# Kernel optimization log

Measured on AMD Instinct MI355X. Metric: run time of the kernel, lower is better.

The kernel has to match this reference:

```python
import jax, jax.numpy as jnp
import numpy as np

DN = ('NCHW', 'OIHW', 'NCHW')


def conv(x, w, s, p):
    return jax.lax.conv_general_dilated(x, w, (s, s), [(p, p), (p, p)], dimension_numbers=DN)


def batchnorm(x, g, b, eps=1e-5):
    # torch BatchNorm2d in training mode: biased batch stats over (N,H,W)
    mu = jnp.mean(x, (0, 2, 3), keepdims=True)
    var = jnp.var(x, (0, 2, 3), keepdims=True)
    return (x - mu) * jax.lax.rsqrt(var + eps) * g.reshape(1, -1, 1, 1) + b.reshape(1, -1, 1, 1)


def pconv(x, mask, W, b, s, p, gb, act):
    # PartialConvLayer.forward
    k = W.shape[-1]
    y = conv(x * mask, W, s, p)
    mc = conv(mask, jnp.ones((1, 1, k, k), x.dtype), s, p)  # all-ones mask conv (frozen)
    zero = mc == 0
    msum = jnp.where(zero, 1.0, mc)
    if b is not None:
        bias = b.reshape(1, -1, 1, 1)
        y = (y - bias) / msum + bias
    else:
        y = y / msum
    y = jnp.where(zero, 0.0, y)
    new_mask = jnp.where(zero, 0.0, 1.0).astype(x.dtype)
    if gb is not None:
        y = batchnorm(y, gb[0], gb[1])
    if act == 'relu':
        y = jax.nn.relu(y)
    elif act == 'leaky':
        y = jnp.where(y >= 0, y, 0.2 * y)
    return y, new_mask


def nlm(mask, feat, h2):
    # Vectorized batch_NLM: Nadaraya-Watson estimator between miss and bkg pixels.
    # Equivalent to the original triple loop: for each miss pixel i,
    #   out[i] = sum_j exp(-||x_i-x_j||^2/h^2) x_j / sum_j exp(-...)   over bkg j.
    # Subtracting the per-row min distance before exp is mathematically identical
    # (the factor cancels in the ratio) and numerically stable.
    bs, C, H, W = feat.shape
    N = H * W
    x = feat.transpose(0, 2, 3, 1).reshape(bs, N, C)
    bkg = mask.reshape(bs, N) > 0.5
    sq = jnp.sum(x * x, -1)  # [bs,N]
    D = jnp.maximum(sq[:, :, None] + sq[:, None, :] - 2.0 * jnp.einsum('bic,bjc->bij', x, x), 0.0)
    Dm = jnp.where(bkg[:, None, :], D, jnp.inf)
    dmin = jnp.min(Dm, -1, keepdims=True)
    w = jnp.where(bkg[:, None, :], jnp.exp(-(D - dmin) / h2), 0.0)
    avg = jnp.einsum('bij,bjc->bic', w, x) / jnp.sum(w, -1, keepdims=True)
    out = jnp.where(bkg[:, :, None], x, avg)  # only miss pixels are replaced
    return out.reshape(bs, H, W, C).transpose(0, 3, 1, 2)


def up2(x):
    return jnp.repeat(jnp.repeat(x, 2, axis=2), 2, axis=3)


def forward(input_x, mask, enc1_W, enc2_W, enc3_W, enc4_W, dec4_W, dec3_W, dec2_W, dec1_W, dec1_b,
            enc2_g, enc2_b, enc3_g, enc3_b, enc4_g, enc4_b,
            dec4_g, dec4_b, dec3_g, dec3_b, dec2_g, dec2_b):
    H_GAUSS2 = 25.0  # h_gaussian = 5
    h0, m0 = input_x, mask
    h1, m1 = pconv(h0, m0, enc1_W, None, 2, 3, None, 'relu')                 # down-7, bn=False
    h2, m2 = pconv(h1, m1, enc2_W, None, 2, 2, (enc2_g, enc2_b), 'relu')     # down-5
    # NLM feature swapping at layer 2 (torch code detaches -> stop_gradient)
    h2 = jax.lax.stop_gradient(nlm(m2, h2, H_GAUSS2))
    buffer_swapped = h2
    h3, m3 = pconv(h2, m2, enc3_W, None, 2, 1, (enc3_g, enc3_b), 'relu')     # down-3
    h4, m4 = pconv(h3, m3, enc4_W, None, 2, 1, (enc4_g, enc4_b), 'relu')     # down-3

    out, omask = h4, m4
    out, omask = up2(out), up2(omask)
    out, omask = pconv(jnp.concatenate([out, h3], 1), omask, dec4_W, None, 1, 1, (dec4_g, dec4_b), 'leaky')
    out, omask = up2(out), up2(omask)
    out, omask = pconv(jnp.concatenate([out, buffer_swapped], 1), omask, dec3_W, None, 1, 1, (dec3_g, dec3_b), 'leaky')
    out, omask = up2(out), up2(omask)
    out, omask = pconv(jnp.concatenate([out, h1], 1), omask, dec2_W, None, 1, 1, (dec2_g, dec2_b), 'leaky')
    out, omask = up2(out), up2(omask)
    out, omask = pconv(jnp.concatenate([out, h0], 1), omask, dec1_W, dec1_b, 1, 1, None, 'none')  # bn=False, bias, no act
    return out


def setup_inputs() -> dict:
    key = jax.random.key(0)
    ks = jax.random.split(key, 12)

    def kaiming(k, shape):
        fan_in = shape[1] * shape[2] * shape[3]
        return jax.random.normal(k, shape, jnp.float32) * np.float32(np.sqrt(2.0 / fan_in))

    bs = 8
    input_x = jax.random.normal(ks[0], (bs, 128, 144, 144), jnp.float32)
    # mask: 1 = background (valid), 0 = missing. Hole large enough to survive two downsamples.
    mask = jnp.ones((bs, 1, 144, 144), jnp.float32).at[:, :, 40:96, 40:96].set(0.0)

    inp = {
        'input_x': input_x,
        'mask': mask,
        'enc1_W': kaiming(ks[1], (256, 128, 7, 7)),
        'enc2_W': kaiming(ks[2], (512, 256, 5, 5)),
        'enc3_W': kaiming(ks[3], (512, 512, 3, 3)),
        'enc4_W': kaiming(ks[4], (512, 512, 3, 3)),
        'dec4_W': kaiming(ks[5], (512, 1024, 3, 3)),
        'dec3_W': kaiming(ks[6], (512, 1024, 3, 3)),
        'dec2_W': kaiming(ks[7], (256, 768, 3, 3)),
        'dec1_W': kaiming(ks[8], (128, 384, 3, 3)),
        'dec1_b': jnp.zeros((128,), jnp.float32),
    }
    for name, c in [('enc2', 512), ('enc3', 512), ('enc4', 512), ('dec4', 512), ('dec3', 512), ('dec2', 256)]:
        inp[name + '_g'] = jnp.ones((c,), jnp.float32)
        inp[name + '_b'] = jnp.zeros((c,), jnp.float32)
    return inp


def reference(input_x, mask, enc1_W, enc2_W, enc3_W, enc4_W, dec4_W, dec3_W, dec2_W, dec1_W, dec1_b,
              enc2_g, enc2_b, enc3_g, enc3_b, enc4_g, enc4_b,
              dec4_g, dec4_b, dec3_g, dec3_b, dec2_g, dec2_b):
    return forward(input_x, mask, enc1_W, enc2_W, enc3_W, enc4_W, dec4_W, dec3_W, dec2_W, dec1_W, dec1_b,
                   enc2_g, enc2_b, enc3_g, enc3_b, enc4_g, enc4_b,
                   dec4_g, dec4_b, dec3_g, dec3_b, dec2_g, dec2_b)
```

## Files before the change

### kernel.cpp

```cpp
#include <hip/hip_runtime.h>
#include <math.h>

#define ACT_NONE 0
#define ACT_RELU 1
#define ACT_LEAKY 2

#define EPI_F32 0
#define EPI_PAIR_RELU 1
#define EPI_F32_BIAS 2

typedef __attribute__((ext_vector_type(8))) short short8;
typedef __attribute__((ext_vector_type(8))) __bf16 bf16x8;
typedef __attribute__((ext_vector_type(4))) float f32x4;
typedef __attribute__((ext_vector_type(4))) unsigned uint4v;

__device__ __forceinline__ float actf(float y, int act) {
    if (act == ACT_RELU)  return y > 0.f ? y : 0.f;
    if (act == ACT_LEAKY) return y >= 0.f ? y : 0.2f * y;
    return y;
}

__device__ __forceinline__ unsigned f2bf_rne(float f) {
    unsigned u = __float_as_uint(f);
    return (u + 0x7FFFu + ((u >> 16) & 1u)) >> 16;
}
__device__ __forceinline__ float bf2f(unsigned h) { return __uint_as_float(h << 16); }
__device__ __forceinline__ unsigned splitpack(float f) {
    unsigned hi = f2bf_rne(f);
    float r = f - bf2f(hi);
    unsigned lo = f2bf_rne(r);
    return (hi & 0xFFFFu) | (lo << 16);
}

__device__ __forceinline__ f32x4 mfma16(short8 a, short8 b, f32x4 c) {
    return __builtin_amdgcn_mfma_f32_16x16x32_bf16(
        __builtin_bit_cast(bf16x8, a), __builtin_bit_cast(bf16x8, b), c, 0, 0, 0);
}

template<int K, int S, bool MHALF>
__global__ void maskconv_kernel(const float* __restrict__ M, int HM, int WM,
                                float* __restrict__ mc, float* __restrict__ nm,
                                int N, int Hin, int Win, int Hout, int Wout) {
    constexpr int P = (K - 1) / 2;
    int idx = blockIdx.x * blockDim.x + threadIdx.x;
    int total = N * Hout * Wout;
    if (idx >= total) return;
    int wo = idx % Wout;
    int t  = idx / Wout;
    int ho = t % Hout;
    int n  = t / Hout;
    float s = 0.f;
    for (int kh = 0; kh < K; ++kh) {
        int ih = ho * S - P + kh;
        if ((unsigned)ih >= (unsigned)Hin) continue;
        const float* mrow = M + ((size_t)n * HM + (MHALF ? (ih >> 1) : ih)) * WM;
        for (int kw = 0; kw < K; ++kw) {
            int iw = wo * S - P + kw;
            if ((unsigned)iw < (unsigned)Win)
                s += mrow[MHALF ? (iw >> 1) : iw];
        }
    }
    mc[idx] = s;
    nm[idx] = (s == 0.f) ? 0.f : 1.f;
}

__global__ void wtransform(const float* __restrict__ W, short* __restrict__ Whi,
                           short* __restrict__ Wlo, int Cout, int Cin, int Ksz,
                           size_t total) {
    size_t idx = (size_t)blockIdx.x * blockDim.x + threadIdx.x;
    if (idx >= total) return;
    int j = (int)(idx & 7);
    int lane = (int)((idx >> 3) & 63);
    size_t r = idx >> 9;
    int COB = Cout >> 4, KB = Cin >> 5;
    int cob = (int)(r % COB); r /= COB;
    int kb = (int)(r % KB);
    int tap = (int)(r / KB);
    int co = cob * 16 + (lane & 15);
    int ci = kb * 32 + (lane >> 4) * 8 + j;
    float f = W[((size_t)co * Cin + ci) * Ksz + tap];
    unsigned hi = f2bf_rne(f);
    float rr = f - bf2f(hi);
    unsigned lo = f2bf_rne(rr);
    Whi[idx] = (short)hi;
    Wlo[idx] = (short)lo;
}

template<int K, int S, int TH, int TW, int NFW, bool AF32, int EPI>
__global__ __launch_bounds__(512) void conv_enc(
    const void* __restrict__ Asrc, int Cin, int Hin, int Win,
    const float* __restrict__ M,
    const short* __restrict__ Whi, const short* __restrict__ Wlo,
    const float* __restrict__ mc, const float* __restrict__ bias,
    void* __restrict__ outp,
    int Hout, int Wout, int Cout, int TX)
{
    static_assert(S == 2, "parity layout assumes stride 2");
    constexpr int P = (K - 1) / 2;
    constexpr int HH  = (TH - 1) * S + K;
    constexpr int HWC = (TW - 1) * S + K;
    constexpr int PXC = HH * HWC;
    constexpr int PW  = (HWC + 1) / 2;
    constexpr int PXC2 = HH * PW * 2;
    __shared__ __align__(16) unsigned BH[4 * PXC2 * 4];
    __shared__ __align__(16) unsigned BL[4 * PXC2 * 4];

    const int t    = threadIdx.x;
    const int lane = t & 63;
    const int wv   = t >> 6;
    const int wm   = wv >> 1;
    const int wn   = wv & 1;
    const int img  = blockIdx.z;
    const int coB  = blockIdx.y * 256;
    const int tile = blockIdx.x;
    const int ty   = tile / TX, tx = tile - ty * TX;
    const int oy0  = ty * TH, ox0 = tx * TW;
    const int KB   = Cin >> 5;
    const int COB  = Cout >> 4;
    const size_t HW = (size_t)Hin * Win;
    const int g  = lane >> 4;
    const int pl = lane & 15;

    f32x4 acc[4][NFW] = {};

#pragma unroll 1
    for (int kb = 0; kb < KB; ++kb) {
        for (int q = t; q < PXC; q += 512) {
            const int r = q / HWC, c = q - r * HWC;
            const int qq = r * PW + (c >> 1) + (c & 1) * (HH * PW);
            const int iy = oy0 * S - P + r;
            const int ix = ox0 * S - P + c;
            bool sel = (unsigned)iy < (unsigned)Hin && (unsigned)ix < (unsigned)Win;
            size_t base = 0;
            if (sel) {
                sel = M[(size_t)img * HW + (size_t)iy * Win + ix] != 0.f;
                base = (size_t)img * Cin * HW + (size_t)iy * Win + ix;
            }
#pragma unroll
            for (int gg = 0; gg < 4; ++gg) {
                const int c0 = kb * 32 + gg * 8;
                unsigned v[8];
#pragma unroll
                for (int j = 0; j < 8; ++j) v[j] = 0u;
                if (sel) {
                    if (AF32) {
                        const float* s = (const float*)Asrc + base + (size_t)c0 * HW;
#pragma unroll
                        for (int j = 0; j < 8; ++j) v[j] = splitpack(s[(size_t)j * HW]);
                    } else {
                        const unsigned* s = (const unsigned*)Asrc + base + (size_t)c0 * HW;
#pragma unroll
                        for (int j = 0; j < 8; ++j) v[j] = s[(size_t)j * HW];
                    }
                }
                uint4v hd, ld;
#pragma unroll
                for (int j = 0; j < 4; ++j) {
                    hd[j] = (v[2 * j] & 0xFFFFu) | (v[2 * j + 1] << 16);
                    ld[j] = (v[2 * j] >> 16) | (v[2 * j + 1] & 0xFFFF0000u);
                }
                *(uint4v*)&BH[(gg * PXC2 + qq) * 4] = hd;
                *(uint4v*)&BL[(gg * PXC2 + qq) * 4] = ld;
            }
        }
        __syncthreads();

#pragma unroll 1
        for (int kh = 0; kh < K; ++kh)
#pragma unroll 1
        for (int kw = 0; kw < K; ++kw) {
            const int tap = kh * K + kw;
            const size_t wb = (((size_t)tap * KB + kb) * COB + (coB >> 4) + wm * 4) * 512
                            + (size_t)lane * 8;
            short8 ah[4], al[4];
#pragma unroll
            for (int fm = 0; fm < 4; ++fm) {
                ah[fm] = *(const short8*)(Whi + wb + (size_t)fm * 512);
                al[fm] = *(const short8*)(Wlo + wb + (size_t)fm * 512);
            }
#pragma unroll
            for (int fn = 0; fn < NFW; ++fn) {
                const int pxf = (wn * NFW + fn) * 16 + pl;
                const int oy = pxf / TW, ox = pxf - oy * TW;
                const int qq = (oy * S + kh) * PW + ox + (kw >> 1) + (kw & 1) * (HH * PW);
                short8 bh = *(const short8*)&BH[(g * PXC2 + qq) * 4];
                short8 bl = *(const short8*)&BL[(g * PXC2 + qq) * 4];
#pragma unroll
                for (int fm = 0; fm < 4; ++fm) {
                    acc[fm][fn] = mfma16(ah[fm], bh, acc[fm][fn]);
                    acc[fm][fn] = mfma16(al[fm], bh, acc[fm][fn]);
                    acc[fm][fn] = mfma16(ah[fm], bl, acc[fm][fn]);
                }
            }
        }
        __syncthreads();
    }

    const int Npix = Hout * Wout;
    const float* mcb = mc + (size_t)img * Npix;
#pragma unroll
    for (int fm = 0; fm < 4; ++fm)
#pragma unroll
    for (int fn = 0; fn < NFW; ++fn) {
        const int co = coB + (wm * 4 + fm) * 16 + (lane >> 4) * 4;
        const int pxf = (wn * NFW + fn) * 16 + (lane & 15);
        const int oy = pxf / TW, ox = pxf - oy * TW;
        const int gy = oy0 + oy, gx = ox0 + ox;
        if (gy >= Hout || gx >= Wout) continue;
        const float m = mcb[(size_t)gy * Wout + gx];
        f32x4 a = acc[fm][fn];
#pragma unroll
        for (int r = 0; r < 4; ++r) {
            float y = a[r];
            if (EPI == EPI_F32_BIAS) {
                const float bv = bias[co + r];
                y = (m == 0.f) ? 0.f : (y - bv) / m + bv;
            } else {
                y = (m == 0.f) ? 0.f : y / m;
            }
            const size_t oidx = ((size_t)img * Cout + co + r) * Npix + (size_t)gy * Wout + gx;
            if (EPI == EPI_PAIR_RELU) {
                y = y > 0.f ? y : 0.f;
                ((unsigned*)outp)[oidx] = splitpack(y);
            } else {
                ((float*)outp)[oidx] = y;
            }
        }
    }
}

template<int TH, int TW, int NFW, bool BF32, int EPI>
__global__ __launch_bounds__(512) void conv3x3(
    const void* __restrict__ Asrc, int CA, int HA, int WA,
    const void* __restrict__ Bsrc, int CB,
    const float* __restrict__ M,
    const short* __restrict__ Whi, const short* __restrict__ Wlo,
    const float* __restrict__ mc, const float* __restrict__ bias,
    void* __restrict__ outp,
    int Hout, int Wout, int Cout, int TX)
{
    constexpr int HALO_H = TH + 2, HALO_W = TW + 2, HALO = HALO_H * HALO_W;
    constexpr int NPIX = TH * TW;
    static_assert(NPIX == 64 * NFW, "tile must be 64*NFW pixels");
    __shared__ __align__(16) unsigned BH[4 * HALO * 4];
    __shared__ __align__(16) unsigned BL[4 * HALO * 4];

    const int t    = threadIdx.x;
    const int lane = t & 63;
    const int wv   = t >> 6;
    const int wm   = wv & 1;
    const int wn   = wv >> 1;
    const int img  = blockIdx.z;
    const int coB  = blockIdx.y * 128;
    const int tile = blockIdx.x;
    const int ty   = tile / TX;
    const int tx   = tile - ty * TX;
    const int oy0  = ty * TH, ox0 = tx * TW;
    const int Cin  = CA + CB;
    const int KB   = Cin >> 5;
    const int COB  = Cout >> 4;
    const int WM   = Wout >> 1;
    const size_t HWA = (size_t)HA * WA;
    const size_t HWB = (size_t)Hout * Wout;

    const int sg = t >> 7;
    const int st = t & 127;
    const int g  = lane >> 4;
    const int pl = lane & 15;

    f32x4 acc[4][NFW] = {};
    const size_t wstride = (size_t)KB * COB * 512;

#pragma unroll 1
    for (int kb = 0; kb < KB; ++kb) {
        for (int q = st; q < HALO; q += 128) {
            const int hy = q / HALO_W, hx = q - hy * HALO_W;
            const int iy = oy0 - 1 + hy, ix = ox0 - 1 + hx;
            bool sel = false;
            size_t abase = 0, bbase = 0;
            if ((unsigned)iy < (unsigned)Hout && (unsigned)ix < (unsigned)Wout) {
                sel = M[((size_t)img * (Hout >> 1) + (iy >> 1)) * WM + (ix >> 1)] != 0.f;
                if (sel) {
                    abase = (size_t)img * CA * HWA + (size_t)(iy >> 1) * WA + (ix >> 1);
                    bbase = (size_t)img * CB * HWB + (size_t)iy * Wout + ix;
                }
            }
            const int c = kb * 32 + sg * 8;
            unsigned v[8];
#pragma unroll
            for (int j = 0; j < 8; ++j) v[j] = 0u;
            if (sel) {
                if (c < CA) {
                    const unsigned* s = (const unsigned*)Asrc + abase + (size_t)c * HWA;
#pragma unroll
                    for (int j = 0; j < 8; ++j) v[j] = s[(size_t)j * HWA];
                } else {
                    if (BF32) {
                        const float* s = (const float*)Bsrc + bbase + (size_t)(c - CA) * HWB;
#pragma unroll
                        for (int j = 0; j < 8; ++j) v[j] = splitpack(s[(size_t)j * HWB]);
                    } else {
                        const unsigned* s = (const unsigned*)Bsrc + bbase + (size_t)(c - CA) * HWB;
#pragma unroll
                        for (int j = 0; j < 8; ++j) v[j] = s[(size_t)j * HWB];
                    }
                }
            }
            uint4v hd, ld;
#pragma unroll
            for (int j = 0; j < 4; ++j) {
                hd[j] = (v[2 * j] & 0xFFFFu) | (v[2 * j + 1] << 16);
                ld[j] = (v[2 * j] >> 16) | (v[2 * j + 1] & 0xFFFF0000u);
            }
            *(uint4v*)&BH[(sg * HALO + q) * 4] = hd;
            *(uint4v*)&BL[(sg * HALO + q) * 4] = ld;
        }
        __syncthreads();

        size_t wb = ((size_t)kb * COB + (coB >> 4) + wm * 4) * 512 + (size_t)lane * 8;
#pragma unroll 1
        for (int tap = 0; tap < 9; ++tap) {
            const int dh = tap / 3, dw = tap - dh * 3;
            short8 ah[4], al[4];
#pragma unroll
            for (int fm = 0; fm < 4; ++fm) {
                ah[fm] = *(const short8*)(Whi + wb + (size_t)fm * 512);
                al[fm] = *(const short8*)(Wlo + wb + (size_t)fm * 512);
            }
#pragma unroll
            for (int fn = 0; fn < NFW; ++fn) {
                const int pxf = (wn * NFW + fn) * 16 + pl;
                const int oy = pxf / TW, ox = pxf - oy * TW;
                const int hpx = (oy + dh) * HALO_W + (ox + dw);
                short8 bh = *(const short8*)&BH[(g * HALO + hpx) * 4];
                short8 bl = *(const short8*)&BL[(g * HALO + hpx) * 4];
#pragma unroll
                for (int fm = 0; fm < 4; ++fm) {
                    acc[fm][fn] = mfma16(ah[fm], bh, acc[fm][fn]);
                    acc[fm][fn] = mfma16(al[fm], bh, acc[fm][fn]);
                    acc[fm][fn] = mfma16(ah[fm], bl, acc[fm][fn]);
                }
            }
            wb += wstride;
        }
        __syncthreads();
    }

    const float* mcb = mc + (size_t)img * HWB;
#pragma unroll
    for (int fm = 0; fm < 4; ++fm)
#pragma unroll
    for (int fn = 0; fn < NFW; ++fn) {
        const int co = coB + (wm * 4 + fm) * 16 + (lane >> 4) * 4;
        const int pxf = (wn * NFW + fn) * 16 + (lane & 15);
        const int oy = pxf / TW, ox = pxf - oy * TW;
        const int gy = oy0 + oy, gx = ox0 + ox;
        if (gy >= Hout || gx >= Wout) continue;
        const float m = mcb[(size_t)gy * Wout + gx];
        f32x4 a = acc[fm][fn];
#pragma unroll
        for (int r = 0; r < 4; ++r) {
            float y = a[r];
            if (EPI == EPI_F32_BIAS) {
                const float bv = bias[co + r];
                y = (m == 0.f) ? 0.f : (y - bv) / m + bv;
            } else {
                y = (m == 0.f) ? 0.f : y / m;
            }
            ((float*)outp)[((size_t)img * Cout + co + r) * HWB + (size_t)gy * Wout + gx] = y;
        }
    }
}

__global__ __launch_bounds__(256) void bn_stats_kernel(const float* __restrict__ y,
                                                       int N, int C, int HW,
                                                       float* __restrict__ mean,
                                                       float* __restrict__ istd) {
    const int c = blockIdx.x;
    double s = 0.0, s2 = 0.0;
    const int tot = N * HW;
    for (int i = threadIdx.x; i < tot; i += blockDim.x) {
        int n = i / HW, hw = i - n * HW;
        float v = y[((size_t)n * C + c) * HW + hw];
        s += v;
        s2 += (double)v * v;
    }
    __shared__ double sh[256], sh2[256];
    sh[threadIdx.x] = s; sh2[threadIdx.x] = s2;
    __syncthreads();
    for (int o = 128; o > 0; o >>= 1) {
        if (threadIdx.x < o) { sh[threadIdx.x] += sh[threadIdx.x + o]; sh2[threadIdx.x] += sh2[threadIdx.x + o]; }
        __syncthreads();
    }
    if (threadIdx.x == 0) {
        double mu = sh[0] / tot;
        double var = sh2[0] / tot - mu * mu;
        mean[c] = (float)mu;
        istd[c] = (float)(1.0 / sqrt(var + 1e-5));
    }
}

__global__ void bn_apply_pair(const float* __restrict__ y,
                              const float* __restrict__ mean, const float* __restrict__ istd,
                              const float* __restrict__ g, const float* __restrict__ b,
                              unsigned* __restrict__ pout, float* __restrict__ fout,
                              int C, int HW, int total, int act) {
    int idx = blockIdx.x * blockDim.x + threadIdx.x;
    if (idx >= total) return;
    int c = (idx / HW) % C;
    float v = (y[idx] - mean[c]) * istd[c] * g[c] + b[c];
    v = actf(v, act);
    pout[idx] = splitpack(v);
    if (fout) fout[idx] = v;
}

#define NLM_C 512
#define NLM_N 1296
#define NLM_MAXM 256
#define NLM_RT 16
#define NLM_KB1 16
#define NLM_KB2 41
#define NLM_PFRAG (NLM_KB1 * NLM_RT * 512)
#define NLM_WFRAG (NLM_KB2 * NLM_RT * 512)

__global__ __launch_bounds__(256) void nlm_trans(const float* __restrict__ h2f,
                                                 unsigned* __restrict__ xTp) {
    __shared__ float tile[32][33];
    const int b = blockIdx.z;
    const int j0 = blockIdx.x * 32, c0 = blockIdx.y * 32;
    const int tx = threadIdx.x & 31, ty = threadIdx.x >> 5;
    for (int cc = ty; cc < 32; cc += 8) {
        const int j = j0 + tx;
        tile[cc][tx] = (j < NLM_N) ? h2f[((size_t)b * NLM_C + c0 + cc) * NLM_N + j] : 0.f;
    }
    __syncthreads();
    for (int jj = ty; jj < 32; jj += 8) {
        const int j = j0 + jj;
        if (j < NLM_N)
            xTp[((size_t)b * NLM_N + j) * NLM_C + c0 + tx] = splitpack(tile[tx][jj]);
    }
}

__global__ void nlm_sq2(const float* __restrict__ h2f, float* __restrict__ sq) {
    const int b = blockIdx.y;
    const int j = blockIdx.x * 256 + threadIdx.x;
    if (j >= NLM_N) return;
    const float* p = h2f + (size_t)b * NLM_C * NLM_N + j;
    float s0 = 0.f, s1 = 0.f, s2 = 0.f, s3 = 0.f;
    for (int c = 0; c < NLM_C; c += 4) {
        float v0 = p[(size_t)c * NLM_N];
        float v1 = p[(size_t)(c + 1) * NLM_N];
        float v2 = p[(size_t)(c + 2) * NLM_N];
        float v3 = p[(size_t)(c + 3) * NLM_N];
        s0 = fmaf(v0, v0, s0); s1 = fmaf(v1, v1, s1);
        s2 = fmaf(v2, v2, s2); s3 = fmaf(v3, v3, s3);
    }
    sq[b * NLM_N + j] = (s0 + s1) + (s2 + s3);
}

__global__ void nlm_compact(const float* __restrict__ nm2, int* __restrict__ list,
                            int* __restrict__ cnt) {
    const int b = blockIdx.x;
    for (int j = threadIdx.x; j < NLM_N; j += 256) {
        if (nm2[(size_t)b * NLM_N + j] == 0.f) {
            int pos = atomicAdd(&cnt[b], 1);
            if (pos < NLM_MAXM) list[b * NLM_MAXM + pos] = j;
        }
    }
}

__global__ void nlm_gather(const unsigned* __restrict__ xTp, const int* __restrict__ list,
                           const int* __restrict__ cnt,
                           short* __restrict__ Phi, short* __restrict__ Plo) {
    const int b = blockIdx.y;
    const int id = blockIdx.x * 256 + threadIdx.x;
    const int i  = id >> 6;
    const int rem = id & 63;
    const int kb = rem >> 2, kg = rem & 3;
    const int lane = kg * 16 + (i & 15), rt = i >> 4;
    const size_t f = (size_t)b * NLM_PFRAG + ((size_t)(kb * NLM_RT + rt) * 64 + lane) * 8;
    if (i < cnt[b]) {
        const int pix = list[b * NLM_MAXM + i];
        const unsigned* s = xTp + ((size_t)b * NLM_N + pix) * NLM_C + kb * 32 + kg * 8;
#pragma unroll
        for (int jj = 0; jj < 8; ++jj) {
            unsigned v = s[jj];
            Phi[f + jj] = (short)(v & 0xFFFFu);
            Plo[f + jj] = (short)(v >> 16);
        }
    } else {
#pragma unroll
        for (int jj = 0; jj < 8; ++jj) { Phi[f + jj] = 0; Plo[f + jj] = 0; }
    }
}

__global__ __launch_bounds__(512) void nlm_gemm1(
    const unsigned* __restrict__ xTp, const short* __restrict__ Phi,
    const short* __restrict__ Plo, const int* __restrict__ cnt,
    float* __restrict__ S) {
    const int img = blockIdx.z, mt = blockIdx.y, nt = blockIdx.x;
    if (mt * 128 >= cnt[img]) return;
    __shared__ __align__(16) unsigned BH[4 * 128 * 4];
    __shared__ __align__(16) unsigned BL[4 * 128 * 4];
    const int t = threadIdx.x, lane = t & 63, wv = t >> 6, wm = wv >> 1, wn = wv & 1;
    const int j0 = nt * 128;
    const int spx = t & 127, sg = t >> 7;
    f32x4 acc[2][4] = {};
#pragma unroll 1
    for (int kb = 0; kb < NLM_KB1; ++kb) {
        unsigned v[8];
#pragma unroll
        for (int jj = 0; jj < 8; ++jj) v[jj] = 0u;
        const int j = j0 + spx;
        if (j < NLM_N) {
            const unsigned* s = xTp + ((size_t)img * NLM_N + j) * NLM_C + kb * 32 + sg * 8;
#pragma unroll
            for (int jj = 0; jj < 8; ++jj) v[jj] = s[jj];
        }
        uint4v hd, ld;
#pragma unroll
        for (int jj = 0; jj < 4; ++jj) {
            hd[jj] = (v[2 * jj] & 0xFFFFu) | (v[2 * jj + 1] << 16);
            ld[jj] = (v[2 * jj] >> 16) | (v[2 * jj + 1] & 0xFFFF0000u);
        }
        *(uint4v*)&BH[(sg * 128 + spx) * 4] = hd;
        *(uint4v*)&BL[(sg * 128 + spx) * 4] = ld;
        __syncthreads();
        const size_t ab = (size_t)img * NLM_PFRAG
                        + (size_t)(kb * NLM_RT + mt * 8 + wm * 2) * 512 + (size_t)lane * 8;
        short8 ah0 = *(const short8*)(Phi + ab);
        short8 ah1 = *(const short8*)(Phi + ab + 512);
        short8 al0 = *(const short8*)(Plo + ab);
        short8 al1 = *(const short8*)(Plo + ab + 512);
        const int g = lane >> 4, pl = lane & 15;
#pragma unroll
        for (int fn = 0; fn < 4; ++fn) {
            const int px = wn * 64 + fn * 16 + pl;
            short8 bh = *(const short8*)&BH[(g * 128 + px) * 4];
            short8 bl = *(const short8*)&BL[(g * 128 + px) * 4];
            acc[0][fn] = mfma16(ah0, bh, acc[0][fn]);
            acc[1][fn] = mfma16(ah1, bh, acc[1][fn]);
            acc[0][fn] = mfma16(al0, bh, acc[0][fn]);
            acc[1][fn] = mfma16(al1, bh, acc[1][fn]);
            acc[0][fn] = mfma16(ah0, bl, acc[0][fn]);
            acc[1][fn] = mfma16(ah1, bl, acc[1][fn]);
        }
        __syncthreads();
    }
#pragma unroll
    for (int fm = 0; fm < 2; ++fm)
#pragma unroll
    for (int fn = 0; fn < 4; ++fn) {
        const int row = mt * 128 + (wm * 2 + fm) * 16 + (lane >> 4) * 4;
        const int j = j0 + wn * 64 + fn * 16 + (lane & 15);
        if (j >= NLM_N) continue;
        f32x4 a = acc[fm][fn];
#pragma unroll
        for (int r = 0; r < 4; ++r)
            S[((size_t)img * NLM_MAXM + row + r) * NLM_N + j] = a[r];
    }
}

__global__ __launch_bounds__(256) void nlm_row(
    const float* __restrict__ S, const float* __restrict__ sq,
    const float* __restrict__ nm2, const int* __restrict__ list,
    const int* __restrict__ cnt,
    short* __restrict__ W2hi, short* __restrict__ W2lo,
    float* __restrict__ sumw, float inv_h2) {
    const int img = blockIdx.y, i = blockIdx.x;
    if (i >= cnt[img] || i >= NLM_MAXM) return;
    __shared__ float Drow[NLM_N];
    __shared__ float red[256];
    const int tid = threadIdx.x;
    const int pix = list[img * NLM_MAXM + i];
    const float sqi = sq[img * NLM_N + pix];
    const float BIG = 3.4e38f;
    float lmin = BIG;
    for (int j = tid; j < NLM_N; j += 256) {
        float d = BIG;
        if (nm2[(size_t)img * NLM_N + j] != 0.f) {
            float dot = S[((size_t)img * NLM_MAXM + i) * NLM_N + j];
            d = sqi + sq[img * NLM_N + j] - 2.f * dot;
            d = d > 0.f ? d : 0.f;
            lmin = d < lmin ? d : lmin;
        }
        Drow[j] = d;
    }
    red[tid] = lmin;
    __syncthreads();
    for (int o = 128; o > 0; o >>= 1) {
        if (tid < o) red[tid] = fminf(red[tid], red[tid + o]);
        __syncthreads();
    }
    const float dmin = red[0];
    __syncthreads();

    const int rt = i >> 4, lr = i & 15;
    float lsum = 0.f;
    for (int j = tid; j < NLM_KB2 * 32; j += 256) {
        float w = 0.f;
        if (j < NLM_N && Drow[j] < 3.3e38f) {
            w = expf(-(Drow[j] - dmin) * inv_h2);
            lsum += w;
        }
        const unsigned u = splitpack(w);
        const int kb = j >> 5, kg = (j & 31) >> 3, jj = j & 7;
        const int lane = kg * 16 + lr;
        const size_t f = (size_t)img * NLM_WFRAG
                       + ((size_t)(kb * NLM_RT + rt) * 64 + lane) * 8 + jj;
        W2hi[f] = (short)(u & 0xFFFFu);
        W2lo[f] = (short)(u >> 16);
    }
    red[tid] = lsum;
    __syncthreads();
    for (int o = 128; o > 0; o >>= 1) {
        if (tid < o) red[tid] += red[tid + o];
        __syncthreads();
    }
    if (tid == 0) sumw[img * NLM_MAXM + i] = red[0];
}

__global__ __launch_bounds__(512) void nlm_gemm2(
    const unsigned* __restrict__ xTp, const short* __restrict__ W2hi,
    const short* __restrict__ W2lo, const int* __restrict__ cnt,
    const float* __restrict__ sumw, const int* __restrict__ list,
    unsigned* __restrict__ out) {
    const int img = blockIdx.z, mt = blockIdx.y, ct = blockIdx.x;
    const int cN = cnt[img] < NLM_MAXM ? cnt[img] : NLM_MAXM;
    if (mt * 128 >= cN) return;
    __shared__ __align__(16) unsigned BH[4 * 128 * 4];
    __shared__ __align__(16) unsigned BL[4 * 128 * 4];
    const int t = threadIdx.x, lane = t & 63, wv = t >> 6, wm = wv >> 1, wn = wv & 1;
    const int c0 = ct * 128;
    const int sc = t & 127, sg = t >> 7;
    f32x4 acc[2][4] = {};
#pragma unroll 1
    for (int kb = 0; kb < NLM_KB2; ++kb) {
        unsigned v[8];
#pragma unroll
        for (int jj = 0; jj < 8; ++jj) {
            const int j = kb * 32 + sg * 8 + jj;
            v[jj] = (j < NLM_N)
                  ? xTp[((size_t)img * NLM_N + j) * NLM_C + c0 + sc] : 0u;
        }
        uint4v hd, ld;
#pragma unroll
        for (int jj = 0; jj < 4; ++jj) {
            hd[jj] = (v[2 * jj] & 0xFFFFu) | (v[2 * jj + 1] << 16);
            ld[jj] = (v[2 * jj] >> 16) | (v[2 * jj + 1] & 0xFFFF0000u);
        }
        *(uint4v*)&BH[(sg * 128 + sc) * 4] = hd;
        *(uint4v*)&BL[(sg * 128 + sc) * 4] = ld;
        __syncthreads();
        const size_t ab = (size_t)img * NLM_WFRAG
                        + (size_t)(kb * NLM_RT + mt * 8 + wm * 2) * 512 + (size_t)lane * 8;
        short8 ah0 = *(const short8*)(W2hi + ab);
        short8 ah1 = *(const short8*)(W2hi + ab + 512);
        short8 al0 = *(const short8*)(W2lo + ab);
        short8 al1 = *(const short8*)(W2lo + ab + 512);
        const int g = lane >> 4, pl = lane & 15;
#pragma unroll
        for (int fn = 0; fn < 4; ++fn) {
            const int px = wn * 64 + fn * 16 + pl;
            short8 bh = *(const short8*)&BH[(g * 128 + px) * 4];
            short8 bl = *(const short8*)&BL[(g * 128 + px) * 4];
            acc[0][fn] = mfma16(ah0, bh, acc[0][fn]);
            acc[1][fn] = mfma16(ah1, bh, acc[1][fn]);
            acc[0][fn] = mfma16(al0, bh, acc[0][fn]);
            acc[1][fn] = mfma16(al1, bh, acc[1][fn]);
            acc[0][fn] = mfma16(ah0, bl, acc[0][fn]);
            acc[1][fn] = mfma16(ah1, bl, acc[1][fn]);
        }
        __syncthreads();
    }
#pragma unroll
    for (int fm = 0; fm < 2; ++fm)
#pragma unroll
    for (int fn = 0; fn < 4; ++fn) {
        const int row = mt * 128 + (wm * 2 + fm) * 16 + (lane >> 4) * 4;
        const int c = c0 + wn * 64 + fn * 16 + (lane & 15);
        f32x4 a = acc[fm][fn];
#pragma unroll
        for (int r = 0; r < 4; ++r) {
            const int ri = row + r;
            if (ri < cN) {
                const float y = a[r] / sumw[img * NLM_MAXM + ri];
                out[((size_t)img * NLM_C + c) * NLM_N + list[img * NLM_MAXM + ri]]
                    = splitpack(y);
            }
        }
    }
}

extern "C" void kernel_launch(void* const* d_in, const int* in_sizes, int n_in,
                              void* d_out, int out_size, void* d_ws, size_t ws_size,
                              hipStream_t stream) {
    const float* x0    = (const float*)d_in[0];
    const float* m0    = (const float*)d_in[1];
    const float* Wsrc[8] = {
        (const float*)d_in[2], (const float*)d_in[3], (const float*)d_in[4],
        (const float*)d_in[5], (const float*)d_in[6], (const float*)d_in[7],
        (const float*)d_in[8], (const float*)d_in[9]
    };
    const float* dec1b = (const float*)d_in[10];
    const float* enc2g = (const float*)d_in[11];
    const float* enc2b = (const float*)d_in[12];
    const float* enc3g = (const float*)d_in[13];
    const float* enc3b = (const float*)d_in[14];
    const float* enc4g = (const float*)d_in[15];
    const float* enc4b = (const float*)d_in[16];
    const float* dec4g = (const float*)d_in[17];
    const float* dec4b = (const float*)d_in[18];
    const float* dec3g = (const float*)d_in[19];
    const float* dec3b = (const float*)d_in[20];
    const float* dec2g = (const float*)d_in[21];
    const float* dec2b = (const float*)d_in[22];
    float* outp = (float*)d_out;

    const int N = 8;
    float* ws = (float*)d_ws;
    size_t off = 0;
    auto alloc = [&](size_t nf) {
        size_t o = off;
        off += ((nf + 63) / 64) * 64;
        return ws + o;
    };

    unsigned* h1pair  = (unsigned*)alloc(10616832);
    unsigned* h2spair = (unsigned*)alloc(5308416);
    unsigned* h3pair  = (unsigned*)alloc(1327104);
    unsigned* h4pair  = (unsigned*)alloc(331776);
    unsigned* d4pair  = (unsigned*)alloc(1327104);
    float* ybuf = alloc(10616832);
    float* h2f  = alloc(5308416);
    unsigned* xTp = (unsigned*)alloc(5308416);
    float* sqb  = alloc(10368);
    float* mc   = alloc(165888);
    float* nm1  = alloc(41472);
    float* nm2  = alloc(10368);
    float* nm3  = alloc(2592);
    float* nm4  = alloc(648);
    float* nmd4 = alloc(2592);
    float* nmd3 = alloc(10368);
    float* nmd2 = alloc(41472);
    float* nmx  = alloc(165888);
    float* bmean = alloc(512);
    float* bistd = alloc(512);
    short* Whi = (short*)alloc(10625024);
    short* Wlo = (short*)alloc(10625024);
    float* Smat = alloc((size_t)8 * NLM_MAXM * NLM_N);
    short* Phi  = (short*)alloc((size_t)8 * NLM_PFRAG / 2);
    short* Plo  = (short*)alloc((size_t)8 * NLM_PFRAG / 2);
    short* W2hi = (short*)alloc((size_t)8 * NLM_WFRAG / 2);
    short* W2lo = (short*)alloc((size_t)8 * NLM_WFRAG / 2);
    int*   mlist = (int*)alloc(8 * NLM_MAXM);
    int*   mcnt  = (int*)alloc(64);
    float* sumw  = alloc(8 * NLM_MAXM);
    unsigned* d3pair = h2spair;
    unsigned* d2pair = h1pair;

    if (ws_size < off * sizeof(float)) return;

    auto cdiv = [](size_t a, size_t b) { return (int)((a + b - 1) / b); };

    struct WLay { int Cout, Cin, K; size_t ofs; };
    const WLay WL[8] = {
        {256, 128, 7, 0},
        {512, 256, 5, 1605632},
        {512, 512, 3, 4882432},
        {512, 512, 3, 7241728},
        {512, 1024, 3, 9601024},
        {512, 1024, 3, 14319616},
        {256, 768, 3, 19038208},
        {128, 384, 3, 20807680},
    };
    for (int i = 0; i < 8; ++i) {
        size_t tot = (size_t)WL[i].Cout * WL[i].Cin * WL[i].K * WL[i].K;
        wtransform<<<cdiv(tot, 256), 256, 0, stream>>>(
            Wsrc[i], Whi + WL[i].ofs, Wlo + WL[i].ofs, WL[i].Cout, WL[i].Cin,
            WL[i].K * WL[i].K, tot);
    }

    maskconv_kernel<7, 2, false><<<cdiv(N * 72 * 72, 256), 256, 0, stream>>>(
        m0, 144, 144, mc, nm1, N, 144, 144, 72, 72);
    conv_enc<7, 2, 8, 8, 2, true, EPI_PAIR_RELU><<<dim3(81, 1, N), 512, 0, stream>>>(
        x0, 128, 144, 144, m0,
        Whi + WL[0].ofs, Wlo + WL[0].ofs, mc, nullptr, h1pair,
        72, 72, 256, 9);

    maskconv_kernel<5, 2, false><<<cdiv(N * 36 * 36, 256), 256, 0, stream>>>(
        nm1, 72, 72, mc, nm2, N, 72, 72, 36, 36);
    conv_enc<5, 2, 8, 8, 2, false, EPI_F32><<<dim3(25, 2, N), 512, 0, stream>>>(
        h1pair, 256, 72, 72, nm1,
        Whi + WL[1].ofs, Wlo + WL[1].ofs, mc, nullptr, ybuf,
        36, 36, 512, 5);
    bn_stats_kernel<<<512, 256, 0, stream>>>(ybuf, N, 512, 1296, bmean, bistd);
    bn_apply_pair<<<cdiv(5308416, 256), 256, 0, stream>>>(
        ybuf, bmean, bistd, enc2g, enc2b, h2spair, h2f, 512, 1296, 5308416, ACT_RELU);

    nlm_trans<<<dim3(41, 16, N), 256, 0, stream>>>(h2f, xTp);
    nlm_sq2<<<dim3(6, N), 256, 0, stream>>>(h2f, sqb);
    hipMemsetAsync(mcnt, 0, 8 * sizeof(int), stream);
    nlm_compact<<<N, 256, 0, stream>>>(nm2, mlist, mcnt);
    nlm_gather<<<dim3(64, N), 256, 0, stream>>>(xTp, mlist, mcnt, Phi, Plo);
    nlm_gemm1<<<dim3(11, 2, N), 512, 0, stream>>>(xTp, Phi, Plo, mcnt, Smat);
    nlm_row<<<dim3(NLM_MAXM, N), 256, 0, stream>>>(Smat, sqb, nm2, mlist, mcnt,
                                                   W2hi, W2lo, sumw, 1.f / 25.f);
    nlm_gemm2<<<dim3(4, 2, N), 512, 0, stream>>>(xTp, W2hi, W2lo, mcnt, sumw,
                                                 mlist, h2spair);

    maskconv_kernel<3, 2, false><<<cdiv(N * 18 * 18, 256), 256, 0, stream>>>(
        nm2, 36, 36, mc, nm3, N, 36, 36, 18, 18);
    conv_enc<3, 2, 4, 8, 1, false, EPI_F32><<<dim3(15, 2, N), 512, 0, stream>>>(
        h2spair, 512, 36, 36, nm2,
        Whi + WL[2].ofs, Wlo + WL[2].ofs, mc, nullptr, ybuf,
        18, 18, 512, 3);
    bn_stats_kernel<<<512, 256, 0, stream>>>(ybuf, N, 512, 324, bmean, bistd);
    bn_apply_pair<<<cdiv(1327104, 256), 256, 0, stream>>>(
        ybuf, bmean, bistd, enc3g, enc3b, h3pair, nullptr, 512, 324, 1327104, ACT_RELU);

    maskconv_kernel<3, 2, false><<<cdiv(N * 9 * 9, 256), 256, 0, stream>>>(
        nm3, 18, 18, mc, nm4, N, 18, 18, 9, 9);
    conv_enc<3, 2, 4, 8, 1, false, EPI_F32><<<dim3(6, 2, N), 512, 0, stream>>>(
        h3pair, 512, 18, 18, nm3,
        Whi + WL[3].ofs, Wlo + WL[3].ofs, mc, nullptr, ybuf,
        9, 9, 512, 2);
    bn_stats_kernel<<<512, 256, 0, stream>>>(ybuf, N, 512, 81, bmean, bistd);
    bn_apply_pair<<<cdiv(331776, 256), 256, 0, stream>>>(
        ybuf, bmean, bistd, enc4g, enc4b, h4pair, nullptr, 512, 81, 331776, ACT_RELU);

    maskconv_kernel<3, 1, true><<<cdiv(N * 18 * 18, 256), 256, 0, stream>>>(
        nm4, 9, 9, mc, nmd4, N, 18, 18, 18, 18);
    conv3x3<8, 8, 1, false, EPI_F32><<<dim3(9, 4, N), 512, 0, stream>>>(
        h4pair, 512, 9, 9, h3pair, 512, nm4,
        Whi + WL[4].ofs, Wlo + WL[4].ofs, mc, nullptr, ybuf,
        18, 18, 512, 3);
    bn_stats_kernel<<<512, 256, 0, stream>>>(ybuf, N, 512, 324, bmean, bistd);
    bn_apply_pair<<<cdiv(1327104, 256), 256, 0, stream>>>(
        ybuf, bmean, bistd, dec4g, dec4b, d4pair, nullptr, 512, 324, 1327104, ACT_LEAKY);

    maskconv_kernel<3, 1, true><<<cdiv(N * 36 * 36, 256), 256, 0, stream>>>(
        nmd4, 18, 18, mc, nmd3, N, 36, 36, 36, 36);
    conv3x3<12, 16, 3, false, EPI_F32><<<dim3(9, 4, N), 512, 0, stream>>>(
        d4pair, 512, 18, 18, h2spair, 512, nmd4,
        Whi + WL[5].ofs, Wlo + WL[5].ofs, mc, nullptr, ybuf,
        36, 36, 512, 3);
    bn_stats_kernel<<<512, 256, 0, stream>>>(ybuf, N, 512, 1296, bmean, bistd);
    bn_apply_pair<<<cdiv(5308416, 256), 256, 0, stream>>>(
        ybuf, bmean, bistd, dec3g, dec3b, d3pair, nullptr, 512, 1296, 5308416, ACT_LEAKY);

    maskconv_kernel<3, 1, true><<<cdiv(N * 72 * 72, 256), 256, 0, stream>>>(
        nmd3, 36, 36, mc, nmd2, N, 72, 72, 72, 72);
    conv3x3<8, 16, 2, false, EPI_F32><<<dim3(45, 2, N), 512, 0, stream>>>(
        d3pair, 512, 36, 36, h1pair, 256, nmd3,
        Whi + WL[6].ofs, Wlo + WL[6].ofs, mc, nullptr, ybuf,
        72, 72, 256, 5);
    bn_stats_kernel<<<256, 256, 0, stream>>>(ybuf, N, 256, 5184, bmean, bistd);
    bn_apply_pair<<<cdiv(10616832, 256), 256, 0, stream>>>(
        ybuf, bmean, bistd, dec2g, dec2b, d2pair, nullptr, 256, 5184, 10616832, ACT_LEAKY);

    maskconv_kernel<3, 1, true><<<cdiv(N * 144 * 144, 256), 256, 0, stream>>>(
        nmd2, 72, 72, mc, nmx, N, 144, 144, 144, 144);
    conv3x3<16, 16, 4, true, EPI_F32_BIAS><<<dim3(81, 1, N), 512, 0, stream>>>(
        d2pair, 256, 72, 72, x0, 128, nmd2,
        Whi + WL[7].ofs, Wlo + WL[7].ofs, mc, dec1b, outp,
        144, 144, 128, 9);
}
```

Measured before the change: 3.031 ms.

## Prefetch next channel block of input halo into registers during MFMA loop

Both conv kernels now compute each thread's halo pixel address and mask test once, outside the channel loop. Each thread then loads the next 32-channel block of the halo into registers while the MFMA taps for the current block run, and writes it to shared memory after the barrier. This is meant to hide global-load latency behind the compute. The dec2 conv also moves to a larger 16x16 tile with four fragments per wave, which gives fewer blocks and more reuse of each halo. The cost is more live registers (up to 32 extra per thread), which may lower occupancy.

```diff
diff --git a/kernel.cpp b/kernel.cpp
--- a/kernel.cpp
+++ b/kernel.cpp
@@ -100,6 +100,7 @@
     constexpr int HH  = (TH - 1) * S + K;
     constexpr int HWC = (TW - 1) * S + K;
     constexpr int PXC = HH * HWC;
+    static_assert(PXC <= 512, "one halo pixel per thread");
     constexpr int PW  = (HWC + 1) / 2;
     constexpr int PXC2 = HH * PW * 2;
     __shared__ __align__(16) unsigned BH[4 * PXC2 * 4];
@@ -121,37 +122,50 @@
     const int g  = lane >> 4;
     const int pl = lane & 15;
 
+    bool sel = false;
+    size_t base = 0;
+    int qq = 0;
+    if (t < PXC) {
+        const int r = t / HWC, c = t - r * HWC;
+        qq = r * PW + (c >> 1) + (c & 1) * (HH * PW);
+        const int iy = oy0 * S - P + r;
+        const int ix = ox0 * S - P + c;
+        if ((unsigned)iy < (unsigned)Hin && (unsigned)ix < (unsigned)Win) {
+            if (M[(size_t)img * HW + (size_t)iy * Win + ix] != 0.f) {
+                sel = true;
+                base = (size_t)img * Cin * HW + (size_t)iy * Win + ix;
+            }
+        }
+    }
+
+    unsigned vr[4][8];
+    auto prefetch = [&](int kb) {
+#pragma unroll
+        for (int gg = 0; gg < 4; ++gg) {
+            const int c0 = kb * 32 + gg * 8;
+#pragma unroll
+            for (int j = 0; j < 8; ++j) vr[gg][j] = 0u;
+            if (sel) {
+                const unsigned* s = (const unsigned*)Asrc + base + (size_t)c0 * HW;
+#pragma unroll
+                for (int j = 0; j < 8; ++j) vr[gg][j] = s[(size_t)j * HW];
+            }
+        }
+    };
+
     f32x4 acc[4][NFW] = {};
+    if (t < PXC) prefetch(0);
 
 #pragma unroll 1
     for (int kb = 0; kb < KB; ++kb) {
-        for (int q = t; q < PXC; q += 512) {
-            const int r = q / HWC, c = q - r * HWC;
-            const int qq = r * PW + (c >> 1) + (c & 1) * (HH * PW);
-            const int iy = oy0 * S - P + r;
-            const int ix = ox0 * S - P + c;
-            bool sel = (unsigned)iy < (unsigned)Hin && (unsigned)ix < (unsigned)Win;
-            size_t base = 0;
-            if (sel) {
-                sel = M[(size_t)img * HW + (size_t)iy * Win + ix] != 0.f;
-                base = (size_t)img * Cin * HW + (size_t)iy * Win + ix;
-            }
+        if (t < PXC) {
 #pragma unroll
             for (int gg = 0; gg < 4; ++gg) {
-                const int c0 = kb * 32 + gg * 8;
                 unsigned v[8];
 #pragma unroll
-                for (int j = 0; j < 8; ++j) v[j] = 0u;
-                if (sel) {
-                    if (AF32) {
-                        const float* s = (const float*)Asrc + base + (size_t)c0 * HW;
-#pragma unroll
-                        for (int j = 0; j < 8; ++j) v[j] = splitpack(s[(size_t)j * HW]);
-                    } else {
-                        const unsigned* s = (const unsigned*)Asrc + base + (size_t)c0 * HW;
-#pragma unroll
-                        for (int j = 0; j < 8; ++j) v[j] = s[(size_t)j * HW];
-                    }
+                for (int j = 0; j < 8; ++j) {
+                    v[j] = vr[gg][j];
+                    if (AF32) v[j] = splitpack(__uint_as_float(v[j]));
                 }
                 uint4v hd, ld;
 #pragma unroll
@@ -164,6 +178,7 @@
             }
         }
         __syncthreads();
+        if (t < PXC && kb + 1 < KB) prefetch(kb + 1);
 
 #pragma unroll 1
         for (int kh = 0; kh < K; ++kh)
@@ -182,9 +197,9 @@
             for (int fn = 0; fn < NFW; ++fn) {
                 const int pxf = (wn * NFW + fn) * 16 + pl;
                 const int oy = pxf / TW, ox = pxf - oy * TW;
-                const int qq = (oy * S + kh) * PW + ox + (kw >> 1) + (kw & 1) * (HH * PW);
-                short8 bh = *(const short8*)&BH[(g * PXC2 + qq) * 4];
-                short8 bl = *(const short8*)&BL[(g * PXC2 + qq) * 4];
+                const int q2 = (oy * S + kh) * PW + ox + (kw >> 1) + (kw & 1) * (HH * PW);
+                short8 bh = *(const short8*)&BH[(g * PXC2 + q2) * 4];
+                short8 bl = *(const short8*)&BL[(g * PXC2 + q2) * 4];
 #pragma unroll
                 for (int fm = 0; fm < 4; ++fm) {
                     acc[fm][fn] = mfma16(ah[fm], bh, acc[fm][fn]);
@@ -241,6 +256,7 @@
 {
     constexpr int HALO_H = TH + 2, HALO_W = TW + 2, HALO = HALO_H * HALO_W;
     constexpr int NPIX = TH * TW;
+    constexpr int SITER = (HALO + 127) / 128;
     static_assert(NPIX == 64 * NFW, "tile must be 64*NFW pixels");
     __shared__ __align__(16) unsigned BH[4 * HALO * 4];
     __shared__ __align__(16) unsigned BL[4 * HALO * 4];
@@ -268,54 +284,76 @@
     const int g  = lane >> 4;
     const int pl = lane & 15;
 
+    bool ssel[SITER];
+    size_t sA[SITER], sB[SITER];
+#pragma unroll
+    for (int i = 0; i < SITER; ++i) {
+        ssel[i] = false; sA[i] = 0; sB[i] = 0;
+        const int q = st + i * 128;
+        if (q < HALO) {
+            const int hy = q / HALO_W, hx = q - hy * HALO_W;
+            const int iy = oy0 - 1 + hy, ix = ox0 - 1 + hx;
+            if ((unsigned)iy < (unsigned)Hout && (unsigned)ix < (unsigned)Wout) {
+                if (M[((size_t)img * (Hout >> 1) + (iy >> 1)) * WM + (ix >> 1)] != 0.f) {
+                    ssel[i] = true;
+                    sA[i] = (size_t)img * CA * HWA + (size_t)(iy >> 1) * WA + (ix >> 1);
+                    sB[i] = (size_t)img * CB * HWB + (size_t)iy * Wout + ix;
+                }
+            }
+        }
+    }
+
+    unsigned vr[SITER][8];
+    auto prefetch = [&](int kb) {
+        const int c = kb * 32 + sg * 8;
+#pragma unroll
+        for (int i = 0; i < SITER; ++i) {
+            const int q = st + i * 128;
+#pragma unroll
+            for (int j = 0; j < 8; ++j) vr[i][j] = 0u;
+            if (q < HALO && ssel[i]) {
+                if (c < CA) {
+                    const unsigned* s = (const unsigned*)Asrc + sA[i] + (size_t)c * HWA;
+#pragma unroll
+                    for (int j = 0; j < 8; ++j) vr[i][j] = s[(size_t)j * HWA];
+                } else {
+                    const unsigned* s = (const unsigned*)Bsrc + sB[i] + (size_t)(c - CA) * HWB;
+#pragma unroll
+                    for (int j = 0; j < 8; ++j) vr[i][j] = s[(size_t)j * HWB];
+                }
+            }
+        }
+    };
+
     f32x4 acc[4][NFW] = {};
     const size_t wstride = (size_t)KB * COB * 512;
+    prefetch(0);
 
 #pragma unroll 1
     for (int kb = 0; kb < KB; ++kb) {
-        for (int q = st; q < HALO; q += 128) {
-            const int hy = q / HALO_W, hx = q - hy * HALO_W;
-            const int iy = oy0 - 1 + hy, ix = ox0 - 1 + hx;
-            bool sel = false;
-            size_t abase = 0, bbase = 0;
-            if ((unsigned)iy < (unsigned)Hout && (unsigned)ix < (unsigned)Wout) {
-                sel = M[((size_t)img * (Hout >> 1) + (iy >> 1)) * WM + (ix >> 1)] != 0.f;
-                if (sel) {
-                    abase = (size_t)img * CA * HWA + (size_t)(iy >> 1) * WA + (ix >> 1);
-                    bbase = (size_t)img * CB * HWB + (size_t)iy * Wout + ix;
+        const bool isB = (kb * 32 + sg * 8) >= CA;
+#pragma unroll
+        for (int i = 0; i < SITER; ++i) {
+            const int q = st + i * 128;
+            if (q < HALO) {
+                unsigned v[8];
+#pragma unroll
+                for (int j = 0; j < 8; ++j) {
+                    v[j] = vr[i][j];
+                    if (BF32 && isB) v[j] = splitpack(__uint_as_float(v[j]));
                 }
-            }
-            const int c = kb * 32 + sg * 8;
-            unsigned v[8];
-#pragma unroll
-            for (int j = 0; j < 8; ++j) v[j] = 0u;
-            if (sel) {
-                if (c < CA) {
-                    const unsigned* s = (const unsigned*)Asrc + abase + (size_t)c * HWA;
-#pragma unroll
-                    for (int j = 0; j < 8; ++j) v[j] = s[(size_t)j * HWA];
-                } else {
-                    if (BF32) {
-                        const float* s = (const float*)Bsrc + bbase + (size_t)(c - CA) * HWB;
-#pragma unroll
-                        for (int j = 0; j < 8; ++j) v[j] = splitpack(s[(size_t)j * HWB]);
-                    } else {
-                        const unsigned* s = (const unsigned*)Bsrc + bbase + (size_t)(c - CA) * HWB;
-#pragma unroll
-                        for (int j = 0; j < 8; ++j) v[j] = s[(size_t)j * HWB];
-                    }
+                uint4v hd, ld;
+#pragma unroll
+                for (int j = 0; j < 4; ++j) {
+                    hd[j] = (v[2 * j] & 0xFFFFu) | (v[2 * j + 1] << 16);
+                    ld[j] = (v[2 * j] >> 16) | (v[2 * j + 1] & 0xFFFF0000u);
                 }
-            }
-            uint4v hd, ld;
-#pragma unroll
-            for (int j = 0; j < 4; ++j) {
-                hd[j] = (v[2 * j] & 0xFFFFu) | (v[2 * j + 1] << 16);
-                ld[j] = (v[2 * j] >> 16) | (v[2 * j + 1] & 0xFFFF0000u);
-            }
-            *(uint4v*)&BH[(sg * HALO + q) * 4] = hd;
-            *(uint4v*)&BL[(sg * HALO + q) * 4] = ld;
-        }
-        __syncthreads();
+                *(uint4v*)&BH[(sg * HALO + q) * 4] = hd;
+                *(uint4v*)&BL[(sg * HALO + q) * 4] = ld;
+            }
+        }
+        __syncthreads();
+        if (kb + 1 < KB) prefetch(kb + 1);
 
         size_t wb = ((size_t)kb * COB + (coB >> 4) + wm * 4) * 512 + (size_t)lane * 8;
 #pragma unroll 1
@@ -851,7 +889,7 @@
 
     maskconv_kernel<3, 1, true><<<cdiv(N * 72 * 72, 256), 256, 0, stream>>>(
         nmd3, 36, 36, mc, nmd2, N, 72, 72, 72, 72);
-    conv3x3<8, 16, 2, false, EPI_F32><<<dim3(45, 2, N), 512, 0, stream>>>(
+    conv3x3<16, 16, 4, false, EPI_F32><<<dim3(25, 2, N), 512, 0, stream>>>(
         d3pair, 512, 36, 36, h1pair, 256, nmd3,
         Whi + WL[6].ofs, Wlo + WL[6].ofs, mc, nullptr, ybuf,
         72, 72, 256, 5);
```

Result: slower. 3.234 ms (+6.7%).
